# Performance work log

Measured on AMD Instinct MI355X. Metric: run time of the kernel, lower is better.

The kernel has to match this reference:

```python
import jax, jax.numpy as jnp
import numpy as np

N = 40962      # icosahedral mesh nodes
E = 245760     # ~degree-6 mesh edges
HD = 256       # hidden_dim
H = 8          # heads
C = HD // H    # out_ch per head = 32
EDIM = 16      # raw edge feature dim
L = 4          # num_layers


def setup_inputs() -> dict:
    key = jax.random.key(0)
    ks = iter(jax.random.split(key, 48))
    def rn(shape, scale=0.05):
        return jax.random.normal(next(ks), shape, dtype=jnp.float32) * scale
    inp = {}
    inp['mesh_enc'] = jax.random.normal(next(ks), (N, HD), dtype=jnp.float32)
    inp['edge_index'] = jax.random.randint(next(ks), (2, E), 0, N)
    inp['edge_attr'] = jax.random.normal(next(ks), (E, EDIM), dtype=jnp.float32)
    # edge input projection
    inp['ep_W'] = rn((EDIM, HD)); inp['ep_b'] = jnp.zeros((HD,), jnp.float32)
    # GATv2 layer 0 (in_ch=HD) and layers 1..L-1 stacked (in_ch=C)
    inp['Wl0'] = rn((HD, H, C));  inp['Wr0'] = rn((HD, H, C))
    inp['Wl'] = rn((L - 1, C, H, C)); inp['Wr'] = rn((L - 1, C, H, C))
    inp['We0'] = rn((HD, H, C));  inp['We'] = rn((L - 1, HD, H, C))
    inp['att0'] = rn((H, C));     inp['att'] = rn((L - 1, H, C))
    inp['Wres0'] = rn((HD, C));   inp['Wres'] = rn((L - 1, C, C))
    inp['bn0'] = jnp.zeros((C,), jnp.float32); inp['bn'] = jnp.zeros((L - 1, C), jnp.float32)
    # edge-update MLP (upd_hidden_dim = hidden_dim * ffn_ratio = HD)
    inp['Wu1_0'] = rn((2 * C + HD, HD)); inp['Wu1'] = rn((L - 1, 2 * C + HD, HD))
    inp['bu1_0'] = jnp.zeros((HD,), jnp.float32); inp['bu1'] = jnp.zeros((L - 1, HD), jnp.float32)
    inp['Wu2_0'] = rn((HD, HD)); inp['Wu2'] = rn((L - 1, HD, HD))
    inp['bu2_0'] = jnp.zeros((HD,), jnp.float32); inp['bu2'] = jnp.zeros((L - 1, HD), jnp.float32)
    # inter-layer LayerNorms (L-1 of them, over C)
    inp['ln_g'] = jnp.ones((L - 1, C), jnp.float32); inp['ln_b'] = jnp.zeros((L - 1, C), jnp.float32)
    # SGFormer-style global branch
    inp['Wq'] = rn((HD, H, C)); inp['Wk'] = rn((HD, H, C)); inp['Wv'] = rn((HD, H, C))
    inp['alpha_p'] = jnp.array(0.5, jnp.float32)
    inp['cn_g'] = jnp.ones((C,), jnp.float32); inp['cn_b'] = jnp.zeros((C,), jnp.float32)
    return inp


def _layernorm(x, g, b):
    mu = x.mean(-1, keepdims=True)
    var = x.var(-1, keepdims=True)
    return (x - mu) / jnp.sqrt(var + 1e-5) * g + b


def _segment_softmax(s, dst, n):
    smax = jax.ops.segment_max(s, dst, num_segments=n)
    smax = jnp.where(jnp.isfinite(smax), smax, 0.0)
    ex = jnp.exp(s - smax[dst])
    den = jax.ops.segment_sum(ex, dst, num_segments=n)
    return ex / (den[dst] + 1e-16)


def _gat(x, e, src, dst, Wl, Wr, We, att, Wres, bn, Wu1, bu1, Wu2, bu2):
    # GATv2 with edge features (PyG semantics), concat=False (head mean), residual
    xl = jnp.einsum('nd,dhc->nhc', x, Wl)          # [N,H,C]
    xr = jnp.einsum('nd,dhc->nhc', x, Wr)
    ee = jnp.einsum('ed,dhc->ehc', e, We)          # [E,H,C]
    m = xl[src] + xr[dst] + ee
    s = jnp.einsum('ehc,hc->eh', jax.nn.leaky_relu(m, 0.2), att)
    a = _segment_softmax(s, dst, x.shape[0])       # [E,H]
    agg = jax.ops.segment_sum(a[:, :, None] * xl[src], dst, num_segments=x.shape[0])
    out = agg.mean(axis=1) + x @ Wres + bn         # [N,C]
    # residual edge update MLP
    h = jnp.concatenate([out[src], out[dst], e], axis=-1)
    e_new = e + jax.nn.gelu(h @ Wu1 + bu1) @ Wu2 + bu2
    return out, e_new


def _sgformer(x, Wq, Wk, Wv):
    # SGFormer linear global attention, O(N)
    q = jnp.einsum('nd,dhc->nhc', x, Wq)
    k = jnp.einsum('nd,dhc->nhc', x, Wk)
    v = jnp.einsum('nd,dhc->nhc', x, Wv)
    qs = q / (jnp.linalg.norm(q, axis=-1, keepdims=True) + 1e-6)
    ks = k / (jnp.linalg.norm(k, axis=-1, keepdims=True) + 1e-6)
    n = jnp.float32(x.shape[0])
    kv = jnp.einsum('nhc,nhd->hcd', ks, v)
    num = jnp.einsum('nhc,hcd->nhd', qs, kv) + n * v
    den = jnp.einsum('nhc,hc->nh', qs, ks.sum(0)) + n
    return (num / den[..., None]).mean(axis=1)     # [N,C]


def reference(mesh_enc, edge_index, edge_attr, ep_W, ep_b, Wl0, Wr0, Wl, Wr, We0, We,
              att0, att, Wres0, Wres, bn0, bn, Wu1_0, Wu1, bu1_0, bu1, Wu2_0, Wu2,
              bu2_0, bu2, ln_g, ln_b, Wq, Wk, Wv, alpha_p, cn_g, cn_b):
    src, dst = edge_index[0], edge_index[1]
    e = edge_attr @ ep_W + ep_b
    x, e = _gat(mesh_enc, e, src, dst, Wl0, Wr0, We0, att0, Wres0, bn0,
                Wu1_0, bu1_0, Wu2_0, bu2_0)
    x = _layernorm(x, ln_g[0], ln_b[0])
    for i in range(L - 1):
        x, e = _gat(x, e, src, dst, Wl[i], Wr[i], We[i], att[i], Wres[i], bn[i],
                    Wu1[i], bu1[i], Wu2[i], bu2[i])
        if i < L - 2:
            x = _layernorm(x, ln_g[i + 1], ln_b[i + 1])
    trans_out = _sgformer(mesh_enc, Wq, Wk, Wv)
    alpha = jax.nn.sigmoid(alpha_p)
    return _layernorm(alpha * x + (1.0 - alpha) * trans_out, cn_g, cn_b)
```

## Files before the change

### kernel.cpp

```cpp
#include <hip/hip_runtime.h>
#include <hip/hip_bf16.h>
#include <math.h>

typedef __hip_bfloat16 bf16;
typedef __attribute__((ext_vector_type(8))) __bf16 bf16x8;
typedef __attribute__((ext_vector_type(4))) float f32x4;

#define NN 40962
#define NE 245760
#define HDIM 256
#define NH 8
#define CH 32

#define MT 64
#define KVB 512

__device__ __forceinline__ float b2f(bf16 v) { return __bfloat162float(v); }
__device__ __forceinline__ bf16 f2b(float v) { return __float2bfloat16(v); }
__device__ __forceinline__ unsigned short f2bs(float v) {
  bf16 b = __float2bfloat16(v);
  return __builtin_bit_cast(unsigned short, b);
}
__device__ __forceinline__ float bs2f(unsigned short u) {
  return __bfloat162float(__builtin_bit_cast(bf16, u));
}

__device__ __forceinline__ float fast_gelu(float x) {
  float x2 = x * x;
  float g = x * (0.7978845608028654f + 0.0356774081f * x2);
  float y = fminf(g * 2.885390081777927f, 60.f);
  float t = exp2f(y);
  float th = (t - 1.f) * __builtin_amdgcn_rcpf(t + 1.f);
  return 0.5f * x * (1.f + th);
}

__global__ __launch_bounds__(512) void k_edge_proj_mfma(
    const float* __restrict__ attr, const int* __restrict__ csre,
    const unsigned short* __restrict__ Weps, const float* __restrict__ bias,
    bf16* __restrict__ e) {
  __shared__ unsigned short At[MT][40];
  __shared__ unsigned short O[MT][264];
  __shared__ int ceS[MT];
  int tid = threadIdx.x, l = tid & 63, w = tid >> 6;
  int lr = l & 15, lk = l >> 4;
  int base = blockIdx.x * MT;
  if (tid < MT) ceS[tid] = csre[base + tid];
  __syncthreads();
  {
    int p = tid >> 3, q = tid & 7;
    if (q < 4) {
      float4 v = *reinterpret_cast<const float4*>(&attr[(size_t)ceS[p] * 16 + q * 4]);
      unsigned short tmp[4] = {f2bs(v.x), f2bs(v.y), f2bs(v.z), f2bs(v.w)};
      *reinterpret_cast<uint2*>(&At[p][q * 4]) = *reinterpret_cast<const uint2*>(tmp);
    } else {
      unsigned short z[4] = {0, 0, 0, 0};
      *reinterpret_cast<uint2*>(&At[p][q * 4]) = *reinterpret_cast<const uint2*>(z);
    }
  }
  __syncthreads();

  int j0 = w * 32;
  f32x4 acc[4][2];
#pragma unroll
  for (int m = 0; m < 4; ++m)
#pragma unroll
    for (int n = 0; n < 2; ++n)
#pragma unroll
      for (int r = 0; r < 4; ++r) acc[m][n][r] = 0.f;
  {
    bf16x8 a[4], b[2];
#pragma unroll
    for (int m = 0; m < 4; ++m)
      a[m] = *reinterpret_cast<const bf16x8*>(&At[m * 16 + lr][lk * 8]);
#pragma unroll
    for (int n = 0; n < 2; ++n) {
      int nt = w * 2 + n;
      b[n] = *reinterpret_cast<const bf16x8*>(Weps + ((size_t)nt * 64 + l) * 8);
    }
#pragma unroll
    for (int m = 0; m < 4; ++m)
#pragma unroll
      for (int n = 0; n < 2; ++n)
        acc[m][n] = __builtin_amdgcn_mfma_f32_16x16x32_bf16(a[m], b[n], acc[m][n], 0, 0, 0);
  }
#pragma unroll
  for (int n = 0; n < 2; ++n) {
    int col = j0 + n * 16 + lr;
    float bv = bias[col];
#pragma unroll
    for (int m = 0; m < 4; ++m)
#pragma unroll
      for (int r = 0; r < 4; ++r)
        O[m * 16 + lk * 4 + r][col] = f2bs(acc[m][n][r] + bv);
  }
  __syncthreads();
  for (int t = tid; t < MT * 32; t += 512) {
    int p = t >> 5, c = t & 31;
    *reinterpret_cast<uint4*>(&e[(size_t)(base + p) * HDIM + c * 8]) =
        *reinterpret_cast<const uint4*>(&O[p][c * 8]);
  }
}

__global__ void k_csr_count(const int* __restrict__ dst, int* __restrict__ cnt) {
  int e = blockIdx.x * 256 + threadIdx.x;
  if (e < NE) atomicAdd(&cnt[dst[e]], 1);
}
__global__ void k_csr_scan(const int* __restrict__ cnt, int* __restrict__ rowptr,
                           int* __restrict__ cursor) {
  __shared__ int part[256];
  __shared__ int tot;
  int t = threadIdx.x;
  const int CHUNK = (NN + 255) / 256;
  int lo = t * CHUNK, hi = lo + CHUNK; if (hi > NN) hi = NN; if (lo > NN) lo = NN;
  int s = 0;
  for (int i = lo; i < hi; ++i) s += cnt[i];
  part[t] = s;
  __syncthreads();
  if (t == 0) {
    int run = 0;
    for (int i = 0; i < 256; ++i) { int v = part[i]; part[i] = run; run += v; }
    tot = run;
  }
  __syncthreads();
  int run = part[t];
  for (int i = lo; i < hi; ++i) { rowptr[i] = run; cursor[i] = run; run += cnt[i]; }
  if (t == 0) rowptr[NN] = tot;
}
__global__ void k_csr_fill(const int* __restrict__ src, const int* __restrict__ dst,
                           int* __restrict__ cursor, int* __restrict__ csre,
                           int* __restrict__ psrc, int* __restrict__ pdst) {
  int e = blockIdx.x * 256 + threadIdx.x;
  if (e >= NE) return;
  int p = atomicAdd(&cursor[dst[e]], 1);
  csre[p] = e;
  psrc[p] = src[e];
  pdst[p] = dst[e];
}

struct SwzP {
  const float *We0, *WeL, *Wl0, *Wr0, *Wq, *Wk, *Wv;
  const float *Wu1_0, *Wu1L, *Wu2_0, *Wu2L, *WlL, *WrL, *epW;
  unsigned short *wall, *w1s, *w2s, *w32s, *wep;
  int* cnt;
};
__device__ __forceinline__ void swz1(const float* __restrict__ W,
                                     unsigned short* __restrict__ out, int t, int Kdiv32) {
  int i = t & 7, l = (t >> 3) & 63;
  int k0 = (t >> 9) % Kdiv32;
  int n0 = t / (512 * Kdiv32);
  int k = k0 * 32 + (l >> 4) * 8 + i;
  int n = n0 * 16 + (l & 15);
  out[t] = f2bs(W[k * 256 + n]);
}
#define SWZ_NW (9 * 65536)
#define SWZ_N1 (3 * 81920)
#define SWZ_N2 (3 * 65536)
#define SWZ_N3 (6 * 8192)
#define SWZ_N4 8192
__global__ void k_swz_fused(SwzP P) {
  int gid = blockIdx.x * 256 + threadIdx.x;
  if (gid < SWZ_NW) {
    int mat = gid >> 16, t = gid & 65535;
    const float* W;
    switch (mat) {
      case 0: W = P.We0; break;
      case 1: W = P.WeL; break;
      case 2: W = P.WeL + 65536; break;
      case 3: W = P.WeL + 131072; break;
      case 4: W = P.Wl0; break;
      case 5: W = P.Wr0; break;
      case 6: W = P.Wq; break;
      case 7: W = P.Wk; break;
      default: W = P.Wv; break;
    }
    swz1(W, P.wall + (size_t)mat * 65536, t, 8);
  } else if (gid < SWZ_NW + SWZ_N1) {
    int idx = gid - SWZ_NW;
    int mat = idx / 81920, t = idx % 81920;
    const float* W = (mat == 0) ? P.Wu1_0 : P.Wu1L + (size_t)(mat - 1) * 81920;
    swz1(W, P.w1s + (size_t)mat * 81920, t, 10);
  } else if (gid < SWZ_NW + SWZ_N1 + SWZ_N2) {
    int idx = gid - SWZ_NW - SWZ_N1;
    int mat = idx >> 16, t = idx & 65535;
    const float* W = (mat == 0) ? P.Wu2_0 : P.Wu2L + (size_t)(mat - 1) * 65536;
    swz1(W, P.w2s + (size_t)mat * 65536, t, 8);
  } else if (gid < SWZ_NW + SWZ_N1 + SWZ_N2 + SWZ_N3) {
    int idx = gid - SWZ_NW - SWZ_N1 - SWZ_N2;
    int mat = idx >> 13, t = idx & 8191;
    int i = mat >> 1;
    const float* W = (mat & 1) ? P.WrL + (size_t)i * 8192 : P.WlL + (size_t)i * 8192;
    swz1(W, P.w32s + (size_t)mat * 8192, t, 1);
  } else if (gid < SWZ_NW + SWZ_N1 + SWZ_N2 + SWZ_N3 + SWZ_N4) {
    int t = gid - (SWZ_NW + SWZ_N1 + SWZ_N2 + SWZ_N3);
    int i = t & 7, l = (t >> 3) & 63;
    int n0 = t >> 9;
    int k = (l >> 4) * 8 + i;
    int n = n0 * 16 + (l & 15);
    P.wep[t] = (k < 16) ? f2bs(P.epW[k * 256 + n]) : (unsigned short)0;
  } else {
    int i = gid - (SWZ_NW + SWZ_N1 + SWZ_N2 + SWZ_N3 + SWZ_N4);
    if (i < NN) P.cnt[i] = 0;
  }
}

__global__ __launch_bounds__(512) void k_edge_score_mfma(
    const bf16* __restrict__ e, const unsigned short* __restrict__ Wes,
    const bf16* __restrict__ xl, const bf16* __restrict__ xr,
    const float* __restrict__ att, const int* __restrict__ psrc,
    const int* __restrict__ pdst, float* __restrict__ sxc) {
  __shared__ unsigned short Ae[MT][264];
  __shared__ float attS[HDIM];
  __shared__ int sidx[MT], didx[MT];
  int tid = threadIdx.x, l = tid & 63, w = tid >> 6;
  int lr = l & 15, lk = l >> 4;
  int base = blockIdx.x * MT;
  if (tid < HDIM) attS[tid] = att[tid];
  if (tid < MT) sidx[tid] = psrc[base + tid];
  else if (tid < 2 * MT) didx[tid - MT] = pdst[base + tid - MT];
  for (int t = tid; t < MT * 32; t += 512) {
    int p = t >> 5, c = t & 31;
    *reinterpret_cast<uint4*>(&Ae[p][c * 8]) =
        *reinterpret_cast<const uint4*>(&e[(size_t)(base + p) * HDIM + c * 8]);
  }
  __syncthreads();

  f32x4 acc[4][2];
#pragma unroll
  for (int m = 0; m < 4; ++m)
#pragma unroll
    for (int n = 0; n < 2; ++n)
#pragma unroll
      for (int r = 0; r < 4; ++r) acc[m][n][r] = 0.f;
  for (int k0 = 0; k0 < 8; ++k0) {
    bf16x8 a[4], b[2];
#pragma unroll
    for (int m = 0; m < 4; ++m)
      a[m] = *reinterpret_cast<const bf16x8*>(&Ae[m * 16 + lr][k0 * 32 + lk * 8]);
#pragma unroll
    for (int n = 0; n < 2; ++n) {
      int nt = w * 2 + n;
      b[n] = *reinterpret_cast<const bf16x8*>(Wes + ((size_t)(nt * 8 + k0) * 64 + l) * 8);
    }
#pragma unroll
    for (int m = 0; m < 4; ++m)
#pragma unroll
      for (int n = 0; n < 2; ++n)
        acc[m][n] = __builtin_amdgcn_mfma_f32_16x16x32_bf16(a[m], b[n], acc[m][n], 0, 0, 0);
  }
  __syncthreads();

#pragma unroll
  for (int n = 0; n < 2; ++n) {
    int col = w * 32 + n * 16 + lr;
    float av = attS[col];
#pragma unroll
    for (int m = 0; m < 4; ++m)
#pragma unroll
      for (int r = 0; r < 4; ++r) {
        int row = m * 16 + lk * 4 + r;
        float xs = b2f(xl[(size_t)sidx[row] * HDIM + col]) +
                   b2f(xr[(size_t)didx[row] * HDIM + col]);
        float mm = acc[m][n][r] + xs;
        mm = (mm > 0.f) ? mm : 0.2f * mm;
        Ae[row][col] = f2bs(mm * av);
      }
  }
  __syncthreads();
  for (int pair = tid; pair < MT * NH; pair += 512) {
    int ed = pair >> 3, h = pair & 7;
    float s = 0.f;
#pragma unroll
    for (int c = 0; c < CH; ++c) s += bs2f(Ae[ed][h * CH + c]);
    sxc[(size_t)(base + ed) * NH + h] = expf(s);
  }
}

#define GCHUNK 64
template <int ID, bool LN>
__global__ __launch_bounds__(256) void k_gat_out(
    const int* __restrict__ rowptr, const int* __restrict__ psrc,
    const float* __restrict__ sxc, const bf16* __restrict__ xl,
    const float* __restrict__ x, const float* __restrict__ Wres,
    const float* __restrict__ bn, const float* __restrict__ lng,
    const float* __restrict__ lnb, float* __restrict__ xpre,
    float* __restrict__ xpost) {
  int n = blockIdx.x;
  int j = threadIdx.x;
  int h = j >> 5, c = j & 31;
  int p0 = rowptr[n], p1 = rowptr[n + 1];
  __shared__ int srcS[GCHUNK];
  __shared__ float exS[GCHUNK * NH];
  float a = 0.f, dsum = 0.f;
  for (int pb = p0; pb < p1; pb += GCHUNK) {
    int chunk = p1 - pb; if (chunk > GCHUNK) chunk = GCHUNK;
    if (j < chunk) srcS[j] = psrc[pb + j];
    for (int t = j; t < chunk * NH; t += 256) exS[t] = sxc[(size_t)pb * NH + t];
    __syncthreads();
    int i = 0;
    for (; i + 4 <= chunk; i += 4) {
      float e0 = exS[(i + 0) * NH + h], e1 = exS[(i + 1) * NH + h];
      float e2 = exS[(i + 2) * NH + h], e3 = exS[(i + 3) * NH + h];
      float x0 = b2f(xl[(size_t)srcS[i + 0] * HDIM + j]);
      float x1 = b2f(xl[(size_t)srcS[i + 1] * HDIM + j]);
      float x2 = b2f(xl[(size_t)srcS[i + 2] * HDIM + j]);
      float x3 = b2f(xl[(size_t)srcS[i + 3] * HDIM + j]);
      a += e0 * x0 + e1 * x1 + e2 * x2 + e3 * x3;
      dsum += e0 + e1 + e2 + e3;
    }
    for (; i < chunk; ++i) {
      float ev = exS[i * NH + h];
      a += ev * b2f(xl[(size_t)srcS[i] * HDIM + j]);
      dsum += ev;
    }
    __syncthreads();
  }
  __shared__ float oh[HDIM];
  __shared__ float rs[NH][CH];
  __shared__ float oc[CH + 1];
  oh[j] = a / (dsum + 1e-16f);
  const int KS = ID / NH;
  float r = 0.f;
  for (int k = h * KS; k < (h + 1) * KS; ++k)
    r += x[(size_t)n * ID + k] * Wres[k * CH + c];
  rs[h][c] = r;
  __syncthreads();
  if (j < CH) {
    float o = 0.f;
#pragma unroll
    for (int hh = 0; hh < NH; ++hh) o += oh[hh * CH + j];
    o *= (1.f / NH);
    float rr = 0.f;
#pragma unroll
    for (int hh = 0; hh < NH; ++hh) rr += rs[hh][j];
    o += rr + bn[j];
    xpre[(size_t)n * CH + j] = o;
    oc[j] = o;
  }
  __syncthreads();
  if (LN && j < CH) {
    float mu = 0.f;
#pragma unroll
    for (int k = 0; k < CH; ++k) mu += oc[k];
    mu *= (1.f / CH);
    float var = 0.f;
#pragma unroll
    for (int k = 0; k < CH; ++k) { float d = oc[k] - mu; var += d * d; }
    var *= (1.f / CH);
    xpost[(size_t)n * CH + j] = (oc[j] - mu) * rsqrtf(var + 1e-5f) * lng[j] + lnb[j];
  }
}

__global__ __launch_bounds__(512) void k_edge_mlp_fused(
    bf16* __restrict__ e, const float* __restrict__ xo,
    const int* __restrict__ psrc, const int* __restrict__ pdst,
    const unsigned short* __restrict__ W1s, const float* __restrict__ bu1,
    const unsigned short* __restrict__ W2s, const float* __restrict__ bu2,
    const unsigned short* __restrict__ Wes2, const float* __restrict__ att2,
    const bf16* __restrict__ xl2, const bf16* __restrict__ xr2,
    float* __restrict__ sxc) {
  __shared__ unsigned short buf[MT][328];
  __shared__ float attS[HDIM];
  __shared__ int sidx[MT], didx[MT];
  int tid = threadIdx.x;
  int l = tid & 63;
  int w = tid >> 6;
  int base = blockIdx.x * MT;
  int lr = l & 15;
  int lk = l >> 4;

  if (tid < HDIM) attS[tid] = att2[tid];
  if (tid < MT) sidx[tid] = psrc[base + tid];
  else if (tid < 2 * MT) didx[tid - MT] = pdst[base + tid - MT];
  __syncthreads();

  for (int t = tid; t < MT * 32; t += 512) {
    int p = t >> 5, cc = t & 31;
    uint4 v = *reinterpret_cast<const uint4*>(&e[(size_t)(base + p) * HDIM + cc * 8]);
    *reinterpret_cast<uint4*>(&buf[p][64 + cc * 8]) = v;
  }
  for (int t = tid; t < MT * 64; t += 512) {
    int p = t >> 6, c = t & 63;
    float v = (c < CH) ? xo[(size_t)sidx[p] * CH + c]
                       : xo[(size_t)didx[p] * CH + (c - CH)];
    buf[p][c] = f2bs(v);
  }
  __syncthreads();

  int j0 = w * 32;

  f32x4 acc[4][2];
#pragma unroll
  for (int m = 0; m < 4; ++m)
#pragma unroll
    for (int n = 0; n < 2; ++n)
#pragma unroll
      for (int r = 0; r < 4; ++r) acc[m][n][r] = 0.f;

  for (int k0 = 0; k0 < 10; ++k0) {
    bf16x8 a[4], b[2];
#pragma unroll
    for (int m = 0; m < 4; ++m)
      a[m] = *reinterpret_cast<const bf16x8*>(&buf[m * 16 + lr][k0 * 32 + lk * 8]);
#pragma unroll
    for (int n = 0; n < 2; ++n) {
      int nt = w * 2 + n;
      b[n] = *reinterpret_cast<const bf16x8*>(W1s + ((size_t)(nt * 10 + k0) * 64 + l) * 8);
    }
#pragma unroll
    for (int m = 0; m < 4; ++m)
#pragma unroll
      for (int n = 0; n < 2; ++n)
        acc[m][n] = __builtin_amdgcn_mfma_f32_16x16x32_bf16(a[m], b[n], acc[m][n], 0, 0, 0);
  }
  __syncthreads();

#pragma unroll
  for (int n = 0; n < 2; ++n) {
    float bv = bu1[j0 + n * 16 + lr];
#pragma unroll
    for (int m = 0; m < 4; ++m)
#pragma unroll
      for (int r = 0; r < 4; ++r) {
        float g = fast_gelu(acc[m][n][r] + bv);
        buf[m * 16 + lk * 4 + r][j0 + n * 16 + lr] = f2bs(g);
      }
  }
  __syncthreads();

#pragma unroll
  for (int m = 0; m < 4; ++m)
#pragma unroll
    for (int n = 0; n < 2; ++n)
#pragma unroll
      for (int r = 0; r < 4; ++r) acc[m][n][r] = 0.f;

  for (int k0 = 0; k0 < 8; ++k0) {
    bf16x8 a[4], b[2];
#pragma unroll
    for (int m = 0; m < 4; ++m)
      a[m] = *reinterpret_cast<const bf16x8*>(&buf[m * 16 + lr][k0 * 32 + lk * 8]);
#pragma unroll
    for (int n = 0; n < 2; ++n) {
      int nt = w * 2 + n;
      b[n] = *reinterpret_cast<const bf16x8*>(W2s + ((size_t)(nt * 8 + k0) * 64 + l) * 8);
    }
#pragma unroll
    for (int m = 0; m < 4; ++m)
#pragma unroll
      for (int n = 0; n < 2; ++n)
        acc[m][n] = __builtin_amdgcn_mfma_f32_16x16x32_bf16(a[m], b[n], acc[m][n], 0, 0, 0);
  }
  __syncthreads();

#pragma unroll
  for (int n = 0; n < 2; ++n) {
    int col = j0 + n * 16 + lr;
    float bv = bu2[col];
#pragma unroll
    for (int m = 0; m < 4; ++m)
#pragma unroll
      for (int r = 0; r < 4; ++r)
        buf[m * 16 + lk * 4 + r][col] = f2bs(acc[m][n][r] + bv);
  }
  __syncthreads();

  for (int t = tid; t < MT * 32; t += 512) {
    int p = t >> 5, cc = t & 31;
    uint4 dv = *reinterpret_cast<const uint4*>(&buf[p][cc * 8]);
    uint4 ev = *reinterpret_cast<const uint4*>(&e[(size_t)(base + p) * HDIM + cc * 8]);
    const unsigned short* dd = (const unsigned short*)&dv;
    const unsigned short* ee = (const unsigned short*)&ev;
    unsigned short ov[8];
#pragma unroll
    for (int i = 0; i < 8; ++i) ov[i] = f2bs(bs2f(ee[i]) + bs2f(dd[i]));
    *reinterpret_cast<uint4*>(&e[(size_t)(base + p) * HDIM + cc * 8]) =
        *reinterpret_cast<const uint4*>(ov);
    *reinterpret_cast<uint4*>(&buf[p][cc * 8]) = *reinterpret_cast<const uint4*>(ov);
  }
  __syncthreads();

#pragma unroll
  for (int m = 0; m < 4; ++m)
#pragma unroll
    for (int n = 0; n < 2; ++n)
#pragma unroll
      for (int r = 0; r < 4; ++r) acc[m][n][r] = 0.f;
  for (int k0 = 0; k0 < 8; ++k0) {
    bf16x8 a[4], b[2];
#pragma unroll
    for (int m = 0; m < 4; ++m)
      a[m] = *reinterpret_cast<const bf16x8*>(&buf[m * 16 + lr][k0 * 32 + lk * 8]);
#pragma unroll
    for (int n = 0; n < 2; ++n) {
      int nt = w * 2 + n;
      b[n] = *reinterpret_cast<const bf16x8*>(Wes2 + ((size_t)(nt * 8 + k0) * 64 + l) * 8);
    }
#pragma unroll
    for (int m = 0; m < 4; ++m)
#pragma unroll
      for (int n = 0; n < 2; ++n)
        acc[m][n] = __builtin_amdgcn_mfma_f32_16x16x32_bf16(a[m], b[n], acc[m][n], 0, 0, 0);
  }
  __syncthreads();

#pragma unroll
  for (int n = 0; n < 2; ++n) {
    int col = j0 + n * 16 + lr;
    float av = attS[col];
#pragma unroll
    for (int m = 0; m < 4; ++m)
#pragma unroll
      for (int r = 0; r < 4; ++r) {
        int row = m * 16 + lk * 4 + r;
        float xs = b2f(xl2[(size_t)sidx[row] * HDIM + col]) +
                   b2f(xr2[(size_t)didx[row] * HDIM + col]);
        float mm = acc[m][n][r] + xs;
        mm = (mm > 0.f) ? mm : 0.2f * mm;
        buf[row][col] = f2bs(mm * av);
      }
  }
  __syncthreads();
  for (int pair = tid; pair < MT * NH; pair += 512) {
    int ed = pair >> 3, h = pair & 7;
    float s = 0.f;
#pragma unroll
    for (int c = 0; c < CH; ++c) s += bs2f(buf[ed][h * CH + c]);
    sxc[(size_t)(base + ed) * NH + h] = expf(s);
  }
}

__global__ __launch_bounds__(256) void k_node_proj0_mfma(
    const float* __restrict__ x, const unsigned short* __restrict__ Wls,
    const unsigned short* __restrict__ Wrs, bf16* __restrict__ xl,
    bf16* __restrict__ xr) {
  __shared__ unsigned short A[MT][264];
  __shared__ unsigned short O[MT][264];
  int tid = threadIdx.x, l = tid & 63, w = tid >> 6;
  int lr = l & 15, lk = l >> 4;
  int base = blockIdx.x * MT;
  for (int t = tid; t < MT * 64; t += 256) {
    int p = t >> 6, c = t & 63;
    int row = base + p; if (row >= NN) row = NN - 1;
    float4 v = *reinterpret_cast<const float4*>(&x[(size_t)row * HDIM + c * 4]);
    unsigned short tmp[4] = {f2bs(v.x), f2bs(v.y), f2bs(v.z), f2bs(v.w)};
    *reinterpret_cast<uint2*>(&A[p][c * 4]) = *reinterpret_cast<const uint2*>(tmp);
  }
  __syncthreads();
  int j0 = w * 64;
#pragma unroll
  for (int mtx = 0; mtx < 2; ++mtx) {
    const unsigned short* Ws = (mtx == 0) ? Wls : Wrs;
    bf16* outp = (mtx == 0) ? xl : xr;
    f32x4 acc[4][4];
#pragma unroll
    for (int m = 0; m < 4; ++m)
#pragma unroll
      for (int n = 0; n < 4; ++n)
#pragma unroll
        for (int r = 0; r < 4; ++r) acc[m][n][r] = 0.f;
    for (int k0 = 0; k0 < 8; ++k0) {
      bf16x8 a[4], b[4];
#pragma unroll
      for (int m = 0; m < 4; ++m)
        a[m] = *reinterpret_cast<const bf16x8*>(&A[m * 16 + lr][k0 * 32 + lk * 8]);
#pragma unroll
      for (int n = 0; n < 4; ++n) {
        int nt = (j0 >> 4) + n;
        b[n] = *reinterpret_cast<const bf16x8*>(Ws + ((size_t)(nt * 8 + k0) * 64 + l) * 8);
      }
#pragma unroll
      for (int m = 0; m < 4; ++m)
#pragma unroll
        for (int n = 0; n < 4; ++n)
          acc[m][n] = __builtin_amdgcn_mfma_f32_16x16x32_bf16(a[m], b[n], acc[m][n], 0, 0, 0);
    }
#pragma unroll
    for (int n = 0; n < 4; ++n)
#pragma unroll
      for (int m = 0; m < 4; ++m)
#pragma unroll
        for (int r = 0; r < 4; ++r)
          O[m * 16 + lk * 4 + r][j0 + n * 16 + lr] = f2bs(acc[m][n][r]);
    __syncthreads();
    for (int t = tid; t < MT * 32; t += 256) {
      int p = t >> 5, c = t & 31;
      if (base + p < NN)
        *reinterpret_cast<uint4*>(&outp[(size_t)(base + p) * HDIM + c * 8]) =
            *reinterpret_cast<const uint4*>(&O[p][c * 8]);
    }
    __syncthreads();
  }
}

__global__ __launch_bounds__(256) void k_node_projS_mfma(
    const float* __restrict__ x, const unsigned short* __restrict__ Wls,
    const unsigned short* __restrict__ Wrs, bf16* __restrict__ xl,
    bf16* __restrict__ xr) {
  __shared__ unsigned short A[MT][40];
  __shared__ unsigned short O[MT][264];
  int tid = threadIdx.x, l = tid & 63, w = tid >> 6;
  int lr = l & 15, lk = l >> 4;
  int base = blockIdx.x * MT;
  for (int t = tid; t < MT * 8; t += 256) {
    int p = t >> 3, q = t & 7;
    int row = base + p; if (row >= NN) row = NN - 1;
    float4 v = *reinterpret_cast<const float4*>(&x[(size_t)row * CH + q * 4]);
    unsigned short tmp[4] = {f2bs(v.x), f2bs(v.y), f2bs(v.z), f2bs(v.w)};
    *reinterpret_cast<uint2*>(&A[p][q * 4]) = *reinterpret_cast<const uint2*>(tmp);
  }
  __syncthreads();
  int j0 = w * 64;
#pragma unroll
  for (int mtx = 0; mtx < 2; ++mtx) {
    const unsigned short* Ws = (mtx == 0) ? Wls : Wrs;
    bf16* outp = (mtx == 0) ? xl : xr;
    f32x4 acc[4][4];
#pragma unroll
    for (int m = 0; m < 4; ++m)
#pragma unroll
      for (int n = 0; n < 4; ++n)
#pragma unroll
        for (int r = 0; r < 4; ++r) acc[m][n][r] = 0.f;
    bf16x8 a[4], b[4];
#pragma unroll
    for (int m = 0; m < 4; ++m)
      a[m] = *reinterpret_cast<const bf16x8*>(&A[m * 16 + lr][lk * 8]);
#pragma unroll
    for (int n = 0; n < 4; ++n) {
      int nt = (j0 >> 4) + n;
      b[n] = *reinterpret_cast<const bf16x8*>(Ws + ((size_t)nt * 64 + l) * 8);
    }
#pragma unroll
    for (int m = 0; m < 4; ++m)
#pragma unroll
      for (int n = 0; n < 4; ++n)
        acc[m][n] = __builtin_amdgcn_mfma_f32_16x16x32_bf16(a[m], b[n], acc[m][n], 0, 0, 0);
#pragma unroll
    for (int n = 0; n < 4; ++n)
#pragma unroll
      for (int m = 0; m < 4; ++m)
#pragma unroll
        for (int r = 0; r < 4; ++r)
          O[m * 16 + lk * 4 + r][j0 + n * 16 + lr] = f2bs(acc[m][n][r]);
    __syncthreads();
    for (int t = tid; t < MT * 32; t += 256) {
      int p = t >> 5, c = t & 31;
      if (base + p < NN)
        *reinterpret_cast<uint4*>(&outp[(size_t)(base + p) * HDIM + c * 8]) =
            *reinterpret_cast<const uint4*>(&O[p][c * 8]);
    }
    __syncthreads();
  }
}

__global__ __launch_bounds__(256) void k_sg_qkv_mfma(
    const float* __restrict__ x, const unsigned short* __restrict__ Wqs,
    const unsigned short* __restrict__ Wks, const unsigned short* __restrict__ Wvs,
    bf16* __restrict__ qs, bf16* __restrict__ ks, bf16* __restrict__ vv) {
  __shared__ unsigned short A[MT][264];
  __shared__ unsigned short O[MT][264];
  int tid = threadIdx.x, l = tid & 63, w = tid >> 6;
  int lr = l & 15, lk = l >> 4;
  int base = blockIdx.x * MT;
  for (int t = tid; t < MT * 64; t += 256) {
    int p = t >> 6, c = t & 63;
    int row = base + p; if (row >= NN) row = NN - 1;
    float4 v = *reinterpret_cast<const float4*>(&x[(size_t)row * HDIM + c * 4]);
    unsigned short tmp[4] = {f2bs(v.x), f2bs(v.y), f2bs(v.z), f2bs(v.w)};
    *reinterpret_cast<uint2*>(&A[p][c * 4]) = *reinterpret_cast<const uint2*>(tmp);
  }
  __syncthreads();
  int j0 = w * 64;
#pragma unroll
  for (int mtx = 0; mtx < 3; ++mtx) {
    const unsigned short* Ws = (mtx == 0) ? Wqs : (mtx == 1) ? Wks : Wvs;
    bf16* outp = (mtx == 0) ? qs : (mtx == 1) ? ks : vv;
    f32x4 acc[4][4];
#pragma unroll
    for (int m = 0; m < 4; ++m)
#pragma unroll
      for (int n = 0; n < 4; ++n)
#pragma unroll
        for (int r = 0; r < 4; ++r) acc[m][n][r] = 0.f;
    for (int k0 = 0; k0 < 8; ++k0) {
      bf16x8 a[4], b[4];
#pragma unroll
      for (int m = 0; m < 4; ++m)
        a[m] = *reinterpret_cast<const bf16x8*>(&A[m * 16 + lr][k0 * 32 + lk * 8]);
#pragma unroll
      for (int n = 0; n < 4; ++n) {
        int nt = (j0 >> 4) + n;
        b[n] = *reinterpret_cast<const bf16x8*>(Ws + ((size_t)(nt * 8 + k0) * 64 + l) * 8);
      }
#pragma unroll
      for (int m = 0; m < 4; ++m)
#pragma unroll
        for (int n = 0; n < 4; ++n)
          acc[m][n] = __builtin_amdgcn_mfma_f32_16x16x32_bf16(a[m], b[n], acc[m][n], 0, 0, 0);
    }
    if (mtx < 2) {
      float pa[4][4], pb[4][4];
#pragma unroll
      for (int m = 0; m < 4; ++m)
#pragma unroll
        for (int r = 0; r < 4; ++r) {
          pa[m][r] = acc[m][0][r] * acc[m][0][r] + acc[m][1][r] * acc[m][1][r];
          pb[m][r] = acc[m][2][r] * acc[m][2][r] + acc[m][3][r] * acc[m][3][r];
        }
#pragma unroll
      for (int off = 1; off < 16; off <<= 1) {
#pragma unroll
        for (int m = 0; m < 4; ++m)
#pragma unroll
          for (int r = 0; r < 4; ++r) {
            pa[m][r] += __shfl_xor(pa[m][r], off);
            pb[m][r] += __shfl_xor(pb[m][r], off);
          }
      }
#pragma unroll
      for (int m = 0; m < 4; ++m)
#pragma unroll
        for (int r = 0; r < 4; ++r) {
          float ra = 1.f / (sqrtf(pa[m][r]) + 1e-6f);
          float rb = 1.f / (sqrtf(pb[m][r]) + 1e-6f);
          acc[m][0][r] *= ra; acc[m][1][r] *= ra;
          acc[m][2][r] *= rb; acc[m][3][r] *= rb;
        }
    }
#pragma unroll
    for (int n = 0; n < 4; ++n)
#pragma unroll
      for (int m = 0; m < 4; ++m)
#pragma unroll
        for (int r = 0; r < 4; ++r)
          O[m * 16 + lk * 4 + r][j0 + n * 16 + lr] = f2bs(acc[m][n][r]);
    __syncthreads();
    for (int t = tid; t < MT * 32; t += 256) {
      int p = t >> 5, c = t & 31;
      if (base + p < NN)
        *reinterpret_cast<uint4*>(&outp[(size_t)(base + p) * HDIM + c * 8]) =
            *reinterpret_cast<const uint4*>(&O[p][c * 8]);
    }
    __syncthreads();
  }
}

__global__ void k_sg_kv1(const bf16* __restrict__ ks, const bf16* __restrict__ vv,
                         float* __restrict__ part) {
  int t = threadIdx.x;
  int h = t >> 5;
  float kvloc[CH];
  float ksl = 0.f;
#pragma unroll
  for (int d = 0; d < CH; ++d) kvloc[d] = 0.f;
  __shared__ float krow[HDIM], vrow[HDIM];
  for (int n = blockIdx.x; n < NN; n += KVB) {
    krow[t] = b2f(ks[(size_t)n * HDIM + t]);
    vrow[t] = b2f(vv[(size_t)n * HDIM + t]);
    __syncthreads();
    float kc = krow[t];
    ksl += kc;
#pragma unroll
    for (int d = 0; d < CH; ++d) kvloc[d] += kc * vrow[h * CH + d];
    __syncthreads();
  }
  float* dstp = part + (size_t)blockIdx.x * 8448;
#pragma unroll
  for (int d = 0; d < CH; d += 4)
    *reinterpret_cast<float4*>(&dstp[t * CH + d]) =
        *reinterpret_cast<const float4*>(&kvloc[d]);
  dstp[8192 + t] = ksl;
}

__global__ void k_sg_kv2(const float* __restrict__ part, float* __restrict__ kv,
                         float* __restrict__ ksum) {
  int idx = blockIdx.x * 256 + threadIdx.x;
  if (idx >= 8448) return;
  float s = 0.f;
  for (int b = 0; b < KVB; ++b) s += part[(size_t)b * 8448 + idx];
  if (idx < 8192) kv[idx] = s;
  else ksum[idx - 8192] = s;
}

__global__ void k_sg_final(const bf16* __restrict__ qs, const bf16* __restrict__ vv,
                           const float* __restrict__ kv, const float* __restrict__ ksum,
                           const float* __restrict__ xg, const float* __restrict__ alphap,
                           const float* __restrict__ cng, const float* __restrict__ cnb,
                           float* __restrict__ out) {
  int t = threadIdx.x;
  int d = t & 31, sub = t >> 5;
  __shared__ float qrow[8][HDIM];
  __shared__ float crow[8][CH];
  int n = blockIdx.x * 8 + sub;
  for (int tt = t; tt < 8 * HDIM; tt += 256) {
    int p = tt >> 8, k = tt & 255;
    int n2 = blockIdx.x * 8 + p;
    if (n2 < NN) qrow[p][k] = b2f(qs[(size_t)n2 * HDIM + k]);
  }
  __syncthreads();
  float alpha = 1.f / (1.f + expf(-alphap[0]));
  const float Nf = (float)NN;
  float comb = 0.f;
  if (n < NN) {
    float acc = 0.f;
#pragma unroll
    for (int h = 0; h < NH; ++h) {
      float nm = 0.f, dp = 0.f;
#pragma unroll 8
      for (int c = 0; c < CH; ++c) {
        float qv = qrow[sub][h * CH + c];
        nm += qv * kv[(h * CH + c) * CH + d];
        dp += qv * ksum[h * CH + c];
      }
      nm += Nf * b2f(vv[(size_t)n * HDIM + h * CH + d]);
      acc += nm / (dp + Nf);
    }
    float trans = acc * (1.f / NH);
    comb = alpha * xg[(size_t)n * CH + d] + (1.f - alpha) * trans;
    crow[sub][d] = comb;
  }
  __syncthreads();
  if (n < NN) {
    float mu = 0.f;
#pragma unroll
    for (int k = 0; k < CH; ++k) mu += crow[sub][k];
    mu *= (1.f / CH);
    float var = 0.f;
#pragma unroll
    for (int k = 0; k < CH; ++k) { float dv = crow[sub][k] - mu; var += dv * dv; }
    var *= (1.f / CH);
    float o = (comb - mu) * rsqrtf(var + 1e-5f) * cng[d] + cnb[d];
    out[(size_t)n * CH + d] = o;
  }
}

extern "C" void kernel_launch(void* const* d_in, const int* in_sizes, int n_in,
                              void* d_out, int out_size, void* d_ws, size_t ws_size,
                              hipStream_t stream) {
  const float* mesh  = (const float*)d_in[0];
  const int*   eidx  = (const int*)d_in[1];
  const float* eattr = (const float*)d_in[2];
  const float* epW   = (const float*)d_in[3];
  const float* epb   = (const float*)d_in[4];
  const float* Wl0   = (const float*)d_in[5];
  const float* Wr0   = (const float*)d_in[6];
  const float* WlL   = (const float*)d_in[7];
  const float* WrL   = (const float*)d_in[8];
  const float* We0   = (const float*)d_in[9];
  const float* WeL   = (const float*)d_in[10];
  const float* att0  = (const float*)d_in[11];
  const float* attL  = (const float*)d_in[12];
  const float* Wres0 = (const float*)d_in[13];
  const float* WresL = (const float*)d_in[14];
  const float* bn0   = (const float*)d_in[15];
  const float* bnL   = (const float*)d_in[16];
  const float* Wu1_0 = (const float*)d_in[17];
  const float* Wu1L  = (const float*)d_in[18];
  const float* bu1_0 = (const float*)d_in[19];
  const float* bu1L  = (const float*)d_in[20];
  const float* Wu2_0 = (const float*)d_in[21];
  const float* Wu2L  = (const float*)d_in[22];
  const float* bu2_0 = (const float*)d_in[23];
  const float* bu2L  = (const float*)d_in[24];
  const float* lng   = (const float*)d_in[25];
  const float* lnb   = (const float*)d_in[26];
  const float* Wq    = (const float*)d_in[27];
  const float* Wk    = (const float*)d_in[28];
  const float* Wv    = (const float*)d_in[29];
  const float* alphap= (const float*)d_in[30];
  const float* cng   = (const float*)d_in[31];
  const float* cnb   = (const float*)d_in[32];

  const int* src = eidx;
  const int* dst = eidx + NE;

  char* base = (char*)d_ws;
  size_t o = 0;
  auto alloc = [&](size_t bytes) -> char* {
    o = (o + 255) & ~(size_t)255;
    char* p = base + o;
    o += bytes;
    return p;
  };
  bf16* e    = (bf16*)alloc((size_t)NE * HDIM * 2);
  bf16* xl   = (bf16*)alloc((size_t)NN * HDIM * 2);
  bf16* xr   = (bf16*)alloc((size_t)NN * HDIM * 2);
  bf16* vvb  = (bf16*)alloc((size_t)NN * HDIM * 2);
  float* sxc = (float*)alloc((size_t)NE * NH * 4);
  float* xa  = (float*)alloc((size_t)NN * CH * 4);
  float* xb  = (float*)alloc((size_t)NN * CH * 4);
  float* xc  = (float*)alloc((size_t)NN * CH * 4);
  float* kv  = (float*)alloc(NH * CH * CH * 4);
  float* ksum= (float*)alloc(NH * CH * 4);
  float* kvpart = (float*)alloc((size_t)KVB * 8448 * 4);
  unsigned short* w1s = (unsigned short*)alloc((size_t)3 * 320 * 256 * 2);
  unsigned short* w2s = (unsigned short*)alloc((size_t)3 * 256 * 256 * 2);
  unsigned short* wall= (unsigned short*)alloc((size_t)9 * 65536 * 2);
  unsigned short* w32s= (unsigned short*)alloc((size_t)6 * 32 * 256 * 2);
  unsigned short* wep = (unsigned short*)alloc((size_t)SWZ_N4 * 2);
  int* cnt    = (int*)alloc((size_t)NN * 4);
  int* rowptr = (int*)alloc((size_t)(NN + 1) * 4);
  int* cursor = (int*)alloc((size_t)NN * 4);
  int* csre   = (int*)alloc((size_t)NE * 4);
  int* psrc   = (int*)alloc((size_t)NE * 4);
  int* pdst   = (int*)alloc((size_t)NE * 4);
  if (ws_size < o) return;

  SwzP P;
  P.We0 = We0; P.WeL = WeL; P.Wl0 = Wl0; P.Wr0 = Wr0; P.Wq = Wq; P.Wk = Wk; P.Wv = Wv;
  P.Wu1_0 = Wu1_0; P.Wu1L = Wu1L; P.Wu2_0 = Wu2_0; P.Wu2L = Wu2L;
  P.WlL = WlL; P.WrL = WrL; P.epW = epW;
  P.wall = wall; P.w1s = w1s; P.w2s = w2s; P.w32s = w32s; P.wep = wep; P.cnt = cnt;
  int swz_total = SWZ_NW + SWZ_N1 + SWZ_N2 + SWZ_N3 + SWZ_N4 + NN;
  k_swz_fused<<<(swz_total + 255) / 256, 256, 0, stream>>>(P);

  k_csr_count<<<(NE + 255) / 256, 256, 0, stream>>>(dst, cnt);
  k_csr_scan<<<1, 256, 0, stream>>>(cnt, rowptr, cursor);
  k_csr_fill<<<(NE + 255) / 256, 256, 0, stream>>>(src, dst, cursor, csre, psrc, pdst);

  k_edge_proj_mfma<<<NE / MT, 512, 0, stream>>>(eattr, csre, wep, epb, e);

  const float* xin = mesh;
  float* post = xb;
  for (int l = 0; l < 4; ++l) {
    const float *Wres_p, *bn_p;
    if (l == 0) { Wres_p = Wres0; bn_p = bn0; }
    else {
      Wres_p = WresL + (size_t)(l - 1) * CH * CH;
      bn_p = bnL + (size_t)(l - 1) * CH;
    }

    if (l == 0) {
      k_node_proj0_mfma<<<(NN + MT - 1) / MT, 256, 0, stream>>>(
          mesh, wall + (size_t)4 * 65536, wall + (size_t)5 * 65536, xl, xr);
      k_edge_score_mfma<<<NE / MT, 512, 0, stream>>>(e, wall, xl, xr, att0,
                                                     psrc, pdst, sxc);
    }

    if (l == 0)
      k_gat_out<HDIM, true><<<NN, 256, 0, stream>>>(rowptr, psrc, sxc, xl, xin, Wres_p,
                                                    bn_p, lng, lnb, xa, post);
    else if (l < 3)
      k_gat_out<CH, true><<<NN, 256, 0, stream>>>(rowptr, psrc, sxc, xl, xin, Wres_p,
                                                  bn_p, lng + (size_t)l * CH,
                                                  lnb + (size_t)l * CH, xa, post);
    else
      k_gat_out<CH, false><<<NN, 256, 0, stream>>>(rowptr, psrc, sxc, xl, xin, Wres_p,
                                                   bn_p, nullptr, nullptr, xa, nullptr);

    if (l < 3) {
      k_node_projS_mfma<<<(NN + MT - 1) / MT, 256, 0, stream>>>(
          post, w32s + (size_t)(l * 2 + 0) * 8192,
          w32s + (size_t)(l * 2 + 1) * 8192, xl, xr);
      k_edge_mlp_fused<<<NE / MT, 512, 0, stream>>>(
          e, xa, psrc, pdst,
          w1s + (size_t)l * 320 * 256, (l == 0) ? bu1_0 : bu1L + (size_t)(l - 1) * HDIM,
          w2s + (size_t)l * 256 * 256, (l == 0) ? bu2_0 : bu2L + (size_t)(l - 1) * HDIM,
          wall + (size_t)(l + 1) * 65536, attL + (size_t)l * HDIM,
          xl, xr, sxc);
    }

    xin = post;
    post = (post == xb) ? xc : xb;
  }

  k_sg_qkv_mfma<<<(NN + MT - 1) / MT, 256, 0, stream>>>(
      mesh, wall + (size_t)6 * 65536, wall + (size_t)7 * 65536,
      wall + (size_t)8 * 65536, xl, xr, vvb);
  k_sg_kv1<<<KVB, 256, 0, stream>>>(xr, vvb, kvpart);
  k_sg_kv2<<<33, 256, 0, stream>>>(kvpart, kv, ksum);
  k_sg_final<<<(NN + 7) / 8, 256, 0, stream>>>(xl, vvb, kv, ksum, xa, alphap, cng, cnb,
                                               (float*)d_out);
}
```

Measured before the change: 1.459 ms.

## Keep edges in original order and scatter scores to CSR positions

Edge features are now stored in original edge order rather than destination-sorted CSR order. Edge kernels read src/dst directly and write only the per-edge attention scores to their CSR slot through a position map, so the gat_out gather stays sorted. This drops the gather through csre in the edge projection and the pdst/csre buffers. In exchange, the per-edge xl/xr gathers by dst lose the locality that sorted order gave them, and the score writes become scattered.

```diff
diff --git a/kernel.cpp b/kernel.cpp
--- a/kernel.cpp
+++ b/kernel.cpp
@@ -35,21 +35,17 @@
 }
 
 __global__ __launch_bounds__(512) void k_edge_proj_mfma(
-    const float* __restrict__ attr, const int* __restrict__ csre,
-    const unsigned short* __restrict__ Weps, const float* __restrict__ bias,
-    bf16* __restrict__ e) {
+    const float* __restrict__ attr, const unsigned short* __restrict__ Weps,
+    const float* __restrict__ bias, bf16* __restrict__ e) {
   __shared__ unsigned short At[MT][40];
   __shared__ unsigned short O[MT][264];
-  __shared__ int ceS[MT];
   int tid = threadIdx.x, l = tid & 63, w = tid >> 6;
   int lr = l & 15, lk = l >> 4;
   int base = blockIdx.x * MT;
-  if (tid < MT) ceS[tid] = csre[base + tid];
-  __syncthreads();
   {
     int p = tid >> 3, q = tid & 7;
     if (q < 4) {
-      float4 v = *reinterpret_cast<const float4*>(&attr[(size_t)ceS[p] * 16 + q * 4]);
+      float4 v = *reinterpret_cast<const float4*>(&attr[(size_t)(base + p) * 16 + q * 4]);
       unsigned short tmp[4] = {f2bs(v.x), f2bs(v.y), f2bs(v.z), f2bs(v.w)};
       *reinterpret_cast<uint2*>(&At[p][q * 4]) = *reinterpret_cast<const uint2*>(tmp);
     } else {
@@ -127,14 +123,13 @@
   if (t == 0) rowptr[NN] = tot;
 }
 __global__ void k_csr_fill(const int* __restrict__ src, const int* __restrict__ dst,
-                           int* __restrict__ cursor, int* __restrict__ csre,
-                           int* __restrict__ psrc, int* __restrict__ pdst) {
+                           int* __restrict__ cursor, int* __restrict__ psrc,
+                           int* __restrict__ pos) {
   int e = blockIdx.x * 256 + threadIdx.x;
   if (e >= NE) return;
   int p = atomicAdd(&cursor[dst[e]], 1);
-  csre[p] = e;
   psrc[p] = src[e];
-  pdst[p] = dst[e];
+  pos[e] = p;
 }
 
 struct SwzP {
@@ -206,8 +201,9 @@
 __global__ __launch_bounds__(512) void k_edge_score_mfma(
     const bf16* __restrict__ e, const unsigned short* __restrict__ Wes,
     const bf16* __restrict__ xl, const bf16* __restrict__ xr,
-    const float* __restrict__ att, const int* __restrict__ psrc,
-    const int* __restrict__ pdst, float* __restrict__ sxc) {
+    const float* __restrict__ att, const int* __restrict__ src,
+    const int* __restrict__ dst, const int* __restrict__ pos,
+    float* __restrict__ sxc) {
   __shared__ unsigned short Ae[MT][264];
   __shared__ float attS[HDIM];
   __shared__ int sidx[MT], didx[MT];
@@ -215,8 +211,8 @@
   int lr = l & 15, lk = l >> 4;
   int base = blockIdx.x * MT;
   if (tid < HDIM) attS[tid] = att[tid];
-  if (tid < MT) sidx[tid] = psrc[base + tid];
-  else if (tid < 2 * MT) didx[tid - MT] = pdst[base + tid - MT];
+  if (tid < MT) sidx[tid] = src[base + tid];
+  else if (tid < 2 * MT) didx[tid - MT] = dst[base + tid - MT];
   for (int t = tid; t < MT * 32; t += 512) {
     int p = t >> 5, c = t & 31;
     *reinterpret_cast<uint4*>(&Ae[p][c * 8]) =
@@ -271,7 +267,7 @@
     float s = 0.f;
 #pragma unroll
     for (int c = 0; c < CH; ++c) s += bs2f(Ae[ed][h * CH + c]);
-    sxc[(size_t)(base + ed) * NH + h] = expf(s);
+    sxc[(size_t)pos[base + ed] * NH + h] = expf(s);
   }
 }
 
@@ -352,7 +348,8 @@
 
 __global__ __launch_bounds__(512) void k_edge_mlp_fused(
     bf16* __restrict__ e, const float* __restrict__ xo,
-    const int* __restrict__ psrc, const int* __restrict__ pdst,
+    const int* __restrict__ src, const int* __restrict__ dst,
+    const int* __restrict__ pos,
     const unsigned short* __restrict__ W1s, const float* __restrict__ bu1,
     const unsigned short* __restrict__ W2s, const float* __restrict__ bu2,
     const unsigned short* __restrict__ Wes2, const float* __restrict__ att2,
@@ -369,8 +366,8 @@
   int lk = l >> 4;
 
   if (tid < HDIM) attS[tid] = att2[tid];
-  if (tid < MT) sidx[tid] = psrc[base + tid];
-  else if (tid < 2 * MT) didx[tid - MT] = pdst[base + tid - MT];
+  if (tid < MT) sidx[tid] = src[base + tid];
+  else if (tid < 2 * MT) didx[tid - MT] = dst[base + tid - MT];
   __syncthreads();
 
   for (int t = tid; t < MT * 32; t += 512) {
@@ -525,7 +522,7 @@
     float s = 0.f;
 #pragma unroll
     for (int c = 0; c < CH; ++c) s += bs2f(buf[ed][h * CH + c]);
-    sxc[(size_t)(base + ed) * NH + h] = expf(s);
+    sxc[(size_t)pos[base + ed] * NH + h] = expf(s);
   }
 }
 
@@ -901,9 +898,8 @@
   int* cnt    = (int*)alloc((size_t)NN * 4);
   int* rowptr = (int*)alloc((size_t)(NN + 1) * 4);
   int* cursor = (int*)alloc((size_t)NN * 4);
-  int* csre   = (int*)alloc((size_t)NE * 4);
   int* psrc   = (int*)alloc((size_t)NE * 4);
-  int* pdst   = (int*)alloc((size_t)NE * 4);
+  int* pos    = (int*)alloc((size_t)NE * 4);
   if (ws_size < o) return;
 
   SwzP P;
@@ -916,9 +912,9 @@
 
   k_csr_count<<<(NE + 255) / 256, 256, 0, stream>>>(dst, cnt);
   k_csr_scan<<<1, 256, 0, stream>>>(cnt, rowptr, cursor);
-  k_csr_fill<<<(NE + 255) / 256, 256, 0, stream>>>(src, dst, cursor, csre, psrc, pdst);
-
-  k_edge_proj_mfma<<<NE / MT, 512, 0, stream>>>(eattr, csre, wep, epb, e);
+  k_csr_fill<<<(NE + 255) / 256, 256, 0, stream>>>(src, dst, cursor, psrc, pos);
+
+  k_edge_proj_mfma<<<NE / MT, 512, 0, stream>>>(eattr, wep, epb, e);
 
   const float* xin = mesh;
   float* post = xb;
@@ -934,7 +930,7 @@
       k_node_proj0_mfma<<<(NN + MT - 1) / MT, 256, 0, stream>>>(
           mesh, wall + (size_t)4 * 65536, wall + (size_t)5 * 65536, xl, xr);
       k_edge_score_mfma<<<NE / MT, 512, 0, stream>>>(e, wall, xl, xr, att0,
-                                                     psrc, pdst, sxc);
+                                                     src, dst, pos, sxc);
     }
 
     if (l == 0)
@@ -953,7 +949,7 @@
           post, w32s + (size_t)(l * 2 + 0) * 8192,
           w32s + (size_t)(l * 2 + 1) * 8192, xl, xr);
       k_edge_mlp_fused<<<NE / MT, 512, 0, stream>>>(
-          e, xa, psrc, pdst,
+          e, xa, src, dst, pos,
           w1s + (size_t)l * 320 * 256, (l == 0) ? bu1_0 : bu1L + (size_t)(l - 1) * HDIM,
           w2s + (size_t)l * 256 * 256, (l == 0) ? bu2_0 : bu2L + (size_t)(l - 1) * HDIM,
           wall + (size_t)(l + 1) * 65536, attL + (size_t)l * HDIM,
```

Result: slower. 1.832 ms (+25.5%).
